# Kernel optimization log

Hardware: AMD Instinct MI355X
Metric: run time of the kernel (lower is better)

Reference implementation:

```python
import jax, jax.numpy as jnp
import numpy as np

B, PD, CD = 8192, 1024, 1024


def setup_inputs() -> dict:
    key = jax.random.key(0)
    ks = jax.random.split(key, 10)
    u = lambda k, shape: jax.random.uniform(k, shape, dtype=jnp.float32, minval=-0.05, maxval=0.05)
    return {
        "P": jax.random.normal(ks[0], (B, PD), dtype=jnp.float32),
        "C1": jax.random.normal(ks[1], (B, CD), dtype=jnp.float32),
        "C2": jax.random.normal(ks[2], (B, CD), dtype=jnp.float32),
        "C3": jax.random.normal(ks[3], (B, CD), dtype=jnp.float32),
        "C4": jax.random.normal(ks[4], (B, CD), dtype=jnp.float32),
        "GateWeight_P": u(ks[5], (PD, CD)),
        "GateWeight_C": u(ks[6], (CD, CD)),
        "GateBias": u(ks[7], (CD,)),
        "OutWeight": u(ks[8], (PD, CD)),
        "OutBias": u(ks[9], (CD, 1)),
    }


def reference(P, C1, C2, C3, C4, GateWeight_P, GateWeight_C, GateBias, OutWeight, OutBias):
    # Stack the 4 choice branches: [4, B, C]
    Cs = jnp.stack([C1, C2, C3, C4], axis=0)
    WP = P @ GateWeight_P                                  # [B, C]
    WC = jnp.einsum("kbc,cd->kbd", Cs, GateWeight_C)       # [4, B, C]
    g = jax.nn.sigmoid(WP[None] + WC + GateBias)           # [4, B, C]
    C_dash = Cs * g                                        # [4, B, C]
    WP_out = P @ OutWeight                                 # [B, C]
    scores = jnp.einsum("kbc,bc->kb", C_dash, WP_out)      # batch_dot axes=[1,1]
    bias = jnp.einsum("kbc,c->kb", C_dash, OutBias[:, 0])  # K.dot(C_dash, OutBias)
    return (scores + bias).T                               # [B, 4]
```

## Files before the change

### kernel.cpp

```cpp
#include <hip/hip_runtime.h>
#include <hip/hip_bf16.h>


#define B_  8192
#define PD_ 1024
#define CD_ 1024

typedef unsigned short ushort_t;
typedef __attribute__((ext_vector_type(8))) short    short8;
typedef __attribute__((ext_vector_type(8))) unsigned short ushort8;
typedef __attribute__((ext_vector_type(4))) float    floatx4;

__device__ __forceinline__ float bf2f(unsigned short u) {
    return __uint_as_float(((unsigned)u) << 16);
}
__device__ __forceinline__ unsigned short f2bf(float f) {
    unsigned u = __float_as_uint(f);
    unsigned r = u + 0x7FFFu + ((u >> 16) & 1u);
    return (unsigned short)(r >> 16);
}

__global__ __launch_bounds__(256) void prep_kernel(const float* __restrict__ P,
                                                   const float* __restrict__ C1,
                                                   const float* __restrict__ C2,
                                                   const float* __restrict__ C3,
                                                   const float* __restrict__ C4,
                                                   const float* __restrict__ GWP,
                                                   const float* __restrict__ OW,
                                                   const float* __restrict__ GWC,
                                                   ushort_t* __restrict__ Pb,
                                                   ushort_t* __restrict__ Call,
                                                   ushort_t* __restrict__ Wcat,
                                                   ushort_t* __restrict__ GWCt,
                                                   float* __restrict__ out) {
    const int bid = blockIdx.x;
    const int tid = threadIdx.x;
    if (bid < 40960) {
        const int seg = bid >> 13;
        const int i   = (bid & 8191) * 256 + tid;
        const float* src;
        ushort_t* dst;
        switch (seg) {
            case 0: src = P;  dst = Pb; break;
            case 1: src = C1; dst = Call; break;
            case 2: src = C2; dst = Call + (size_t)1 * B_ * CD_; break;
            case 3: src = C3; dst = Call + (size_t)2 * B_ * CD_; break;
            default: src = C4; dst = Call + (size_t)3 * B_ * CD_; break;
        }
        float4 v = ((const float4*)src)[i];
        ushort4 o;
        o.x = f2bf(v.x); o.y = f2bf(v.y); o.z = f2bf(v.z); o.w = f2bf(v.w);
        ((ushort4*)dst)[i] = o;
    } else if (bid < 44032) {
        __shared__ float tile[32][33];
        const int tb  = bid - 40960;
        const int seg = tb >> 10;
        const int t32 = tb & 1023;
        const float* src;
        ushort_t* dst;
        switch (seg) {
            case 0: src = GWP; dst = Wcat; break;
            case 1: src = OW;  dst = Wcat + 1024 * 1024; break;
            default: src = GWC; dst = GWCt; break;
        }
        const int c0 = (t32 & 31) * 32, r0 = (t32 >> 5) * 32;
        const int x = tid & 31, y = tid >> 5;
        for (int i = y; i < 32; i += 8)
            tile[i][x] = src[(size_t)(r0 + i) * 1024 + c0 + x];
        __syncthreads();
        for (int i = y; i < 32; i += 8)
            dst[(size_t)(c0 + i) * 1024 + r0 + x] = f2bf(tile[x][i]);
    } else {
        const int i = (bid - 44032) * 256 + tid;
        ((float4*)out)[i] = float4{0.f, 0.f, 0.f, 0.f};
    }
}

__device__ __forceinline__ void gl_lds16(const void* g, void* l) {
    __builtin_amdgcn_global_load_lds((const __attribute__((address_space(1))) void*)g,
                                     (__attribute__((address_space(3))) void*)l, 16, 0, 0);
}

__global__ __launch_bounds__(512, 4) void gemmA(const ushort_t* __restrict__ A,
                                                const ushort_t* __restrict__ Bt,
                                                ushort_t* __restrict__ C) {
    __shared__ ushort_t smem[12288];
    ushort_t* lA = smem;
    ushort_t* lB = smem + 4096;
    const int K = 1024, N = 2048;
    const int xcd = blockIdx.x & 7, q = blockIdx.x >> 3;
    const int tileM = ((q >> 3) * 8 + xcd) * 128;
    const int tileN = (q & 7) * 256;

    const int t = threadIdx.x;
    const int wave = t >> 6, lane = t & 63;
    const int quad = lane >> 4, l16 = lane & 15;
    const int wm = wave >> 2, wn = wave & 3;

    const int srow = lane >> 2;
    const int sc   = ((lane & 3) ^ ((lane >> 4) & 3)) * 8;
    const ushort_t* Ag  = A  + (size_t)(tileM + wave * 16 + srow) * K + sc;
    const ushort_t* Bg0 = Bt + (size_t)(tileN + wave * 32 + srow) * K + sc;
    const ushort_t* Bg1 = Bg0 + (size_t)16 * K;
    const int loA = wave * 512 + lane * 8;
    const int loB = wave * 1024 + lane * 8;
    const int fro = (l16 * 4 + (quad ^ (l16 >> 2))) * 8;

    floatx4 acc[4][4];
#pragma unroll
    for (int i = 0; i < 4; i++)
#pragma unroll
        for (int j = 0; j < 4; j++) acc[i][j] = (floatx4)0.f;

    for (int k0 = 0; k0 < K; k0 += 32) {
        gl_lds16(Ag + k0,  &lA[loA]);
        gl_lds16(Bg0 + k0, &lB[loB]);
        gl_lds16(Bg1 + k0, &lB[loB + 512]);
        __syncthreads();
        short8 af[4], bfr[4];
#pragma unroll
        for (int mi = 0; mi < 4; mi++)
            af[mi] = *(const short8*)&lA[(wm * 4 + mi) * 512 + fro];
#pragma unroll
        for (int ni = 0; ni < 4; ni++)
            bfr[ni] = *(const short8*)&lB[(wn * 4 + ni) * 512 + fro];
#pragma unroll
        for (int mi = 0; mi < 4; mi++)
#pragma unroll
            for (int ni = 0; ni < 4; ni++)
                acc[mi][ni] = __builtin_amdgcn_mfma_f32_16x16x32_bf16(
                    af[mi], bfr[ni], acc[mi][ni], 0, 0, 0);
        __syncthreads();
    }
#pragma unroll
    for (int mi = 0; mi < 4; mi++)
#pragma unroll
        for (int ni = 0; ni < 4; ni++)
#pragma unroll
            for (int r = 0; r < 4; r++) {
                int row = tileM + wm * 64 + mi * 16 + quad * 4 + r;
                int col = tileN + wn * 64 + ni * 16 + l16;
                C[(size_t)row * N + col] = f2bf(acc[mi][ni][r]);
            }
}

__global__ __launch_bounds__(512, 4) void gemmB_fused(const ushort_t* __restrict__ Call,
                                                      const ushort_t* __restrict__ GWCt,
                                                      const ushort_t* __restrict__ WPcat,
                                                      const float* __restrict__ Gb,
                                                      const float* __restrict__ Ob,
                                                      float* __restrict__ out) {
    __shared__ ushort_t smem[12288];
    ushort_t* lA = smem;
    ushort_t* lB = smem + 4096;
    const int K = 1024;
    const int xcd = blockIdx.x & 7, q = blockIdx.x >> 3;
    const int tileM = ((q >> 2) * 8 + xcd) * 128;
    const int tileN = (q & 3) * 256;

    const int t = threadIdx.x;
    const int wave = t >> 6, lane = t & 63;
    const int quad = lane >> 4, l16 = lane & 15;
    const int wm = wave >> 2, wn = wave & 3;

    const int srow = lane >> 2;
    const int sc   = ((lane & 3) ^ ((lane >> 4) & 3)) * 8;
    const ushort_t* Ag  = Call + (size_t)(tileM + wave * 16 + srow) * K + sc;
    const ushort_t* Bg0 = GWCt + (size_t)(tileN + wave * 32 + srow) * K + sc;
    const ushort_t* Bg1 = Bg0 + (size_t)16 * K;
    const int loA = wave * 512 + lane * 8;
    const int loB = wave * 1024 + lane * 8;
    const int fro = (l16 * 4 + (quad ^ (l16 >> 2))) * 8;

    floatx4 acc[4][4];
#pragma unroll
    for (int i = 0; i < 4; i++)
#pragma unroll
        for (int j = 0; j < 4; j++) acc[i][j] = (floatx4)0.f;

    for (int k0 = 0; k0 < K; k0 += 32) {
        gl_lds16(Ag + k0,  &lA[loA]);
        gl_lds16(Bg0 + k0, &lB[loB]);
        gl_lds16(Bg1 + k0, &lB[loB + 512]);
        __syncthreads();
        short8 af[4], bfr[4];
#pragma unroll
        for (int mi = 0; mi < 4; mi++)
            af[mi] = *(const short8*)&lA[(wm * 4 + mi) * 512 + fro];
#pragma unroll
        for (int ni = 0; ni < 4; ni++)
            bfr[ni] = *(const short8*)&lB[(wn * 4 + ni) * 512 + fro];
#pragma unroll
        for (int mi = 0; mi < 4; mi++)
#pragma unroll
            for (int ni = 0; ni < 4; ni++)
                acc[mi][ni] = __builtin_amdgcn_mfma_f32_16x16x32_bf16(
                    af[mi], bfr[ni], acc[mi][ni], 0, 0, 0);
        __syncthreads();
    }

    const int kk   = tileM >> 13;
    const int b0   = (tileM & 8191) + wm * 64 + quad * 4;
    const int rowg = tileM + wm * 64 + quad * 4;

#pragma unroll
    for (int mi = 0; mi < 4; mi++) {
        float part[4] = {0.f, 0.f, 0.f, 0.f};
#pragma unroll
        for (int ni = 0; ni < 4; ni++) {
            const int gcol = tileN + wn * 64 + ni * 16 + l16;
            const float gbv = Gb[gcol];
            const float obv = Ob[gcol];
            const ushort_t* wpp = WPcat + (size_t)(b0 + mi * 16) * 2048 + gcol;
            const ushort_t* ckp = Call  + (size_t)(rowg + mi * 16) * 1024 + gcol;
#pragma unroll
            for (int r = 0; r < 4; r++) {
                float wp  = bf2f(wpp[(size_t)r * 2048]);
                float wpo = bf2f(wpp[(size_t)r * 2048 + 1024]);
                float ck  = bf2f(ckp[(size_t)r * 1024]);
                float x = wp + acc[mi][ni][r] + gbv;
                float g = 1.f / (1.f + __expf(-x));
                part[r] += ck * g * (wpo + obv);
            }
        }
#pragma unroll
        for (int r = 0; r < 4; r++) {
            part[r] += __shfl_xor(part[r], 1);
            part[r] += __shfl_xor(part[r], 2);
            part[r] += __shfl_xor(part[r], 4);
            part[r] += __shfl_xor(part[r], 8);
        }
        if (l16 == 0) {
#pragma unroll
            for (int r = 0; r < 4; r++)
                atomicAdd(&out[(size_t)(b0 + mi * 16 + r) * 4 + kk], part[r]);
        }
    }
}

extern "C" void kernel_launch(void* const* d_in, const int* in_sizes, int n_in,
                              void* d_out, int out_size, void* d_ws, size_t ws_size,
                              hipStream_t stream) {
    (void)in_sizes; (void)n_in; (void)out_size; (void)ws_size;
    const float* P   = (const float*)d_in[0];
    const float* C1  = (const float*)d_in[1];
    const float* C2  = (const float*)d_in[2];
    const float* C3  = (const float*)d_in[3];
    const float* C4  = (const float*)d_in[4];
    const float* GWP = (const float*)d_in[5];
    const float* GWC = (const float*)d_in[6];
    const float* Gb  = (const float*)d_in[7];
    const float* OW  = (const float*)d_in[8];
    const float* Ob  = (const float*)d_in[9];
    float* out = (float*)d_out;

    char* ws = (char*)d_ws;
    ushort_t* Pb    = (ushort_t*)(ws);
    ushort_t* Call  = (ushort_t*)(ws + (16u << 20));
    ushort_t* Wcat  = (ushort_t*)(ws + (80u << 20));
    ushort_t* GWCt  = (ushort_t*)(ws + (84u << 20));
    ushort_t* WPcat = (ushort_t*)(ws + (86u << 20));

    prep_kernel<<<44064, 256, 0, stream>>>(P, C1, C2, C3, C4, GWP, OW, GWC,
                                           Pb, Call, Wcat, GWCt, out);
    gemmA<<<512, 512, 0, stream>>>(Pb, Wcat, WPcat);
    gemmB_fused<<<1024, 512, 0, stream>>>(Call, GWCt, WPcat, Gb, Ob, out);
}
```

Before: 345.0 us.

## Use 256x256 tiles with 4-stage LDS pipeline and interleaved WP pairs

Replaces both GEMMs' 128x256 single-buffered K loop with a shared 256x256 tile routine. It prefetches three K-steps ahead into a 4-slot LDS ring, using vmcnt waits and a single barrier per step, and raises MFMA priority during compute. gemmA now writes WP and WP_out interleaved so the fused epilogue reads one 32-bit word per element instead of two strided loads, and bias loads are hoisted. Larger tiles raise data reuse but halve the number of blocks, lower occupancy to 2 blocks per CU and increase register pressure.

Measured after the change: 356.9 us. +3.5%, slower.

```diff
diff --git a/kernel.cpp b/kernel.cpp
--- a/kernel.cpp
+++ b/kernel.cpp
@@ -7,8 +7,8 @@
 #define CD_ 1024
 
 typedef unsigned short ushort_t;
+typedef unsigned int   uint_t;
 typedef __attribute__((ext_vector_type(8))) short    short8;
-typedef __attribute__((ext_vector_type(8))) unsigned short ushort8;
 typedef __attribute__((ext_vector_type(4))) float    floatx4;
 
 __device__ __forceinline__ float bf2f(unsigned short u) {
@@ -81,146 +81,155 @@
                                      (__attribute__((address_space(3))) void*)l, 16, 0, 0);
 }
 
-__global__ __launch_bounds__(512, 4) void gemmA(const ushort_t* __restrict__ A,
-                                                const ushort_t* __restrict__ Bt,
-                                                ushort_t* __restrict__ C) {
-    __shared__ ushort_t smem[12288];
-    ushort_t* lA = smem;
-    ushort_t* lB = smem + 4096;
-    const int K = 1024, N = 2048;
+#define VM8()  asm volatile("s_waitcnt vmcnt(8)" ::: "memory")
+#define VM4()  asm volatile("s_waitcnt vmcnt(4)" ::: "memory")
+#define VM0()  asm volatile("s_waitcnt vmcnt(0)" ::: "memory")
+#define BARR() __builtin_amdgcn_s_barrier()
+
+__device__ __forceinline__ void gemm256_pipeline(const ushort_t* __restrict__ A,
+                                                 const ushort_t* __restrict__ Bt,
+                                                 int tileM, int tileN,
+                                                 ushort_t* smem,
+                                                 floatx4 (&acc)[8][4]) {
+    const int K = 1024;
+    const int t = threadIdx.x;
+    const int w = t >> 6, lane = t & 63;
+    const int quad = lane >> 4, l16 = lane & 15;
+    const int wm = w >> 2, wn = w & 3;
+
+    const int segg = ((lane & 3) ^ ((lane >> 3) & 3)) * 8;
+    const ushort_t* Ap0 = A  + (size_t)(tileM + w * 16 + (lane >> 2)) * K + segg;
+    const ushort_t* Ap1 = Ap0 + (size_t)128 * K;
+    const ushort_t* Bp0 = Bt + (size_t)(tileN + w * 16 + (lane >> 2)) * K + segg;
+    const ushort_t* Bp1 = Bp0 + (size_t)128 * K;
+    const int lA0 = w * 512 + lane * 8;
+    const int lA1 = lA0 + 4096;
+    const int lB0 = 8192 + lA0;
+    const int lB1 = lB0 + 4096;
+
+    const int xs  = (quad ^ ((l16 >> 1) & 3)) * 8;
+    const int roA = (wm * 128 + l16) * 32 + xs;
+    const int roB = 8192 + (wn * 64 + l16) * 32 + xs;
+
+#pragma unroll
+    for (int i = 0; i < 8; i++)
+#pragma unroll
+        for (int j = 0; j < 4; j++) acc[i][j] = (floatx4)0.f;
+
+#define STAGE(kt) do {                                                       \
+        const int base_ = ((kt) & 3) * 16384; const int k0_ = (kt) * 32;     \
+        gl_lds16(Ap0 + k0_, &smem[base_ + lA0]);                             \
+        gl_lds16(Ap1 + k0_, &smem[base_ + lA1]);                             \
+        gl_lds16(Bp0 + k0_, &smem[base_ + lB0]);                             \
+        gl_lds16(Bp1 + k0_, &smem[base_ + lB1]); } while (0)
+
+#define COMPUTE(kt) do {                                                     \
+        const int base_ = ((kt) & 3) * 16384;                                \
+        short8 af_[8], bf_[4];                                               \
+        _Pragma("unroll")                                                    \
+        for (int mi = 0; mi < 8; mi++)                                       \
+            af_[mi] = *(const short8*)&smem[base_ + roA + mi * 512];         \
+        _Pragma("unroll")                                                    \
+        for (int ni = 0; ni < 4; ni++)                                       \
+            bf_[ni] = *(const short8*)&smem[base_ + roB + ni * 512];         \
+        __builtin_amdgcn_s_setprio(1);                                       \
+        _Pragma("unroll")                                                    \
+        for (int mi = 0; mi < 8; mi++)                                       \
+        _Pragma("unroll")                                                    \
+        for (int ni = 0; ni < 4; ni++)                                       \
+            acc[mi][ni] = __builtin_amdgcn_mfma_f32_16x16x32_bf16(           \
+                af_[mi], bf_[ni], acc[mi][ni], 0, 0, 0);                     \
+        __builtin_amdgcn_s_setprio(0); } while (0)
+
+    STAGE(0); STAGE(1); STAGE(2);
+#pragma unroll 4
+    for (int kt = 0; kt < 28; ++kt) {
+        VM8(); BARR();
+        STAGE(kt + 3);
+        COMPUTE(kt);
+    }
+    VM8(); BARR(); STAGE(31); COMPUTE(28);
+    VM8(); BARR(); COMPUTE(29);
+    VM4(); BARR(); COMPUTE(30);
+    VM0(); BARR(); COMPUTE(31);
+#undef STAGE
+#undef COMPUTE
+}
+
+__global__ __launch_bounds__(512, 2) void gemmA_k(const ushort_t* __restrict__ A,
+                                                  const ushort_t* __restrict__ Bt,
+                                                  ushort_t* __restrict__ C) {
+    __shared__ ushort_t smem[65536];
     const int xcd = blockIdx.x & 7, q = blockIdx.x >> 3;
-    const int tileM = ((q >> 3) * 8 + xcd) * 128;
+    const int tileM = ((q >> 3) * 8 + xcd) * 256;
     const int tileN = (q & 7) * 256;
 
-    const int t = threadIdx.x;
-    const int wave = t >> 6, lane = t & 63;
-    const int quad = lane >> 4, l16 = lane & 15;
-    const int wm = wave >> 2, wn = wave & 3;
-
-    const int srow = lane >> 2;
-    const int sc   = ((lane & 3) ^ ((lane >> 4) & 3)) * 8;
-    const ushort_t* Ag  = A  + (size_t)(tileM + wave * 16 + srow) * K + sc;
-    const ushort_t* Bg0 = Bt + (size_t)(tileN + wave * 32 + srow) * K + sc;
-    const ushort_t* Bg1 = Bg0 + (size_t)16 * K;
-    const int loA = wave * 512 + lane * 8;
-    const int loB = wave * 1024 + lane * 8;
-    const int fro = (l16 * 4 + (quad ^ (l16 >> 2))) * 8;
-
-    floatx4 acc[4][4];
-#pragma unroll
-    for (int i = 0; i < 4; i++)
-#pragma unroll
-        for (int j = 0; j < 4; j++) acc[i][j] = (floatx4)0.f;
-
-    for (int k0 = 0; k0 < K; k0 += 32) {
-        gl_lds16(Ag + k0,  &lA[loA]);
-        gl_lds16(Bg0 + k0, &lB[loB]);
-        gl_lds16(Bg1 + k0, &lB[loB + 512]);
-        __syncthreads();
-        short8 af[4], bfr[4];
-#pragma unroll
-        for (int mi = 0; mi < 4; mi++)
-            af[mi] = *(const short8*)&lA[(wm * 4 + mi) * 512 + fro];
-#pragma unroll
-        for (int ni = 0; ni < 4; ni++)
-            bfr[ni] = *(const short8*)&lB[(wn * 4 + ni) * 512 + fro];
-#pragma unroll
-        for (int mi = 0; mi < 4; mi++)
-#pragma unroll
-            for (int ni = 0; ni < 4; ni++)
-                acc[mi][ni] = __builtin_amdgcn_mfma_f32_16x16x32_bf16(
-                    af[mi], bfr[ni], acc[mi][ni], 0, 0, 0);
-        __syncthreads();
-    }
-#pragma unroll
-    for (int mi = 0; mi < 4; mi++)
-#pragma unroll
-        for (int ni = 0; ni < 4; ni++)
+    floatx4 acc[8][4];
+    gemm256_pipeline(A, Bt, tileM, tileN, smem, acc);
+
+    const int t = threadIdx.x, lane = t & 63, quad = lane >> 4, l16 = lane & 15;
+    const int w = t >> 6, wm = w >> 2, wn = w & 3;
+    const int rowb = tileM + wm * 128 + quad * 4;
+#pragma unroll
+    for (int mi = 0; mi < 8; mi++)
+#pragma unroll
+        for (int ni = 0; ni < 4; ni++) {
+            const int col = tileN + wn * 64 + ni * 16 + l16;
+            const int ci = col & 1023, hi = col >> 10;
 #pragma unroll
             for (int r = 0; r < 4; r++) {
-                int row = tileM + wm * 64 + mi * 16 + quad * 4 + r;
-                int col = tileN + wn * 64 + ni * 16 + l16;
-                C[(size_t)row * N + col] = f2bf(acc[mi][ni][r]);
+                const int row = rowb + mi * 16 + r;
+                C[(size_t)(row * 1024 + ci) * 2 + hi] = f2bf(acc[mi][ni][r]);
             }
-}
-
-__global__ __launch_bounds__(512, 4) void gemmB_fused(const ushort_t* __restrict__ Call,
+        }
+}
+
+__global__ __launch_bounds__(512, 2) void gemmB_fused(const ushort_t* __restrict__ Call,
                                                       const ushort_t* __restrict__ GWCt,
-                                                      const ushort_t* __restrict__ WPcat,
+                                                      const uint_t* __restrict__ WPcat,
                                                       const float* __restrict__ Gb,
                                                       const float* __restrict__ Ob,
                                                       float* __restrict__ out) {
-    __shared__ ushort_t smem[12288];
-    ushort_t* lA = smem;
-    ushort_t* lB = smem + 4096;
-    const int K = 1024;
+    __shared__ ushort_t smem[65536];
     const int xcd = blockIdx.x & 7, q = blockIdx.x >> 3;
-    const int tileM = ((q >> 2) * 8 + xcd) * 128;
+    const int tileM = ((q >> 2) * 8 + xcd) * 256;
     const int tileN = (q & 3) * 256;
 
-    const int t = threadIdx.x;
-    const int wave = t >> 6, lane = t & 63;
-    const int quad = lane >> 4, l16 = lane & 15;
-    const int wm = wave >> 2, wn = wave & 3;
-
-    const int srow = lane >> 2;
-    const int sc   = ((lane & 3) ^ ((lane >> 4) & 3)) * 8;
-    const ushort_t* Ag  = Call + (size_t)(tileM + wave * 16 + srow) * K + sc;
-    const ushort_t* Bg0 = GWCt + (size_t)(tileN + wave * 32 + srow) * K + sc;
-    const ushort_t* Bg1 = Bg0 + (size_t)16 * K;
-    const int loA = wave * 512 + lane * 8;
-    const int loB = wave * 1024 + lane * 8;
-    const int fro = (l16 * 4 + (quad ^ (l16 >> 2))) * 8;
-
-    floatx4 acc[4][4];
-#pragma unroll
-    for (int i = 0; i < 4; i++)
-#pragma unroll
-        for (int j = 0; j < 4; j++) acc[i][j] = (floatx4)0.f;
-
-    for (int k0 = 0; k0 < K; k0 += 32) {
-        gl_lds16(Ag + k0,  &lA[loA]);
-        gl_lds16(Bg0 + k0, &lB[loB]);
-        gl_lds16(Bg1 + k0, &lB[loB + 512]);
-        __syncthreads();
-        short8 af[4], bfr[4];
-#pragma unroll
-        for (int mi = 0; mi < 4; mi++)
-            af[mi] = *(const short8*)&lA[(wm * 4 + mi) * 512 + fro];
-#pragma unroll
-        for (int ni = 0; ni < 4; ni++)
-            bfr[ni] = *(const short8*)&lB[(wn * 4 + ni) * 512 + fro];
-#pragma unroll
-        for (int mi = 0; mi < 4; mi++)
-#pragma unroll
-            for (int ni = 0; ni < 4; ni++)
-                acc[mi][ni] = __builtin_amdgcn_mfma_f32_16x16x32_bf16(
-                    af[mi], bfr[ni], acc[mi][ni], 0, 0, 0);
-        __syncthreads();
-    }
-
-    const int kk   = tileM >> 13;
-    const int b0   = (tileM & 8191) + wm * 64 + quad * 4;
-    const int rowg = tileM + wm * 64 + quad * 4;
-
-#pragma unroll
-    for (int mi = 0; mi < 4; mi++) {
+    floatx4 acc[8][4];
+    gemm256_pipeline(Call, GWCt, tileM, tileN, smem, acc);
+
+    const int t = threadIdx.x, lane = t & 63, quad = lane >> 4, l16 = lane & 15;
+    const int w = t >> 6, wm = w >> 2, wn = w & 3;
+
+    const int kk    = tileM >> 13;
+    const int b0    = (tileM & 8191) + wm * 128 + quad * 4;
+    const int rowg0 = tileM + wm * 128 + quad * 4;
+
+    float gbv[4], obv[4];
+    int   gcol[4];
+#pragma unroll
+    for (int ni = 0; ni < 4; ni++) {
+        gcol[ni] = tileN + wn * 64 + ni * 16 + l16;
+        gbv[ni]  = Gb[gcol[ni]];
+        obv[ni]  = Ob[gcol[ni]];
+    }
+
+#pragma unroll
+    for (int mi = 0; mi < 8; mi++) {
         float part[4] = {0.f, 0.f, 0.f, 0.f};
 #pragma unroll
         for (int ni = 0; ni < 4; ni++) {
-            const int gcol = tileN + wn * 64 + ni * 16 + l16;
-            const float gbv = Gb[gcol];
-            const float obv = Ob[gcol];
-            const ushort_t* wpp = WPcat + (size_t)(b0 + mi * 16) * 2048 + gcol;
-            const ushort_t* ckp = Call  + (size_t)(rowg + mi * 16) * 1024 + gcol;
+            const uint_t*   wpp = WPcat + (size_t)(b0 + mi * 16) * 1024 + gcol[ni];
+            const ushort_t* ckp = Call  + (size_t)(rowg0 + mi * 16) * 1024 + gcol[ni];
 #pragma unroll
             for (int r = 0; r < 4; r++) {
-                float wp  = bf2f(wpp[(size_t)r * 2048]);
-                float wpo = bf2f(wpp[(size_t)r * 2048 + 1024]);
-                float ck  = bf2f(ckp[(size_t)r * 1024]);
-                float x = wp + acc[mi][ni][r] + gbv;
-                float g = 1.f / (1.f + __expf(-x));
-                part[r] += ck * g * (wpo + obv);
+                const uint_t wpair = wpp[(size_t)r * 1024];
+                const float wp  = bf2f((unsigned short)(wpair & 0xffffu));
+                const float wpo = bf2f((unsigned short)(wpair >> 16));
+                const float ck  = bf2f(ckp[(size_t)r * 1024]);
+                const float x = wp + acc[mi][ni][r] + gbv[ni];
+                const float g = 1.f / (1.f + __expf(-x));
+                part[r] += ck * g * (wpo + obv[ni]);
             }
         }
 #pragma unroll
@@ -263,6 +272,6 @@
 
     prep_kernel<<<44064, 256, 0, stream>>>(P, C1, C2, C3, C4, GWP, OW, GWC,
                                            Pb, Call, Wcat, GWCt, out);
-    gemmA<<<512, 512, 0, stream>>>(Pb, Wcat, WPcat);
-    gemmB_fused<<<1024, 512, 0, stream>>>(Call, GWCt, WPcat, Gb, Ob, out);
-}
+    gemmA_k<<<256, 512, 0, stream>>>(Pb, Wcat, WPcat);
+    gemmB_fused<<<512, 512, 0, stream>>>(Call, GWCt, (const uint_t*)WPcat, Gb, Ob, out);
+}
```

## Interleave WP/WPout outputs as bf16 pairs and retune LDS swizzle

Applied to the files above, without the earlier changes.

gemmA now writes WP and WP_out interleaved per column, so the fused epilogue of gemmB reads both values with a single 32-bit load instead of two scattered 16-bit loads. The LDS XOR swizzle used for global-to-LDS staging and fragment reads changes to a different lane-bit pattern to reduce bank conflicts. Bias loads are hoisted out of the mi loop. The interleaved stores in gemmA become strided 2-byte writes, which may coalesce less well.

New measurement: 345.4 us. About the same (+0.1%).

```diff
diff --git a/kernel.cpp b/kernel.cpp
--- a/kernel.cpp
+++ b/kernel.cpp
@@ -7,8 +7,8 @@
 #define CD_ 1024
 
 typedef unsigned short ushort_t;
+typedef unsigned int   uint_t;
 typedef __attribute__((ext_vector_type(8))) short    short8;
-typedef __attribute__((ext_vector_type(8))) unsigned short ushort8;
 typedef __attribute__((ext_vector_type(4))) float    floatx4;
 
 __device__ __forceinline__ float bf2f(unsigned short u) {
@@ -87,7 +87,7 @@
     __shared__ ushort_t smem[12288];
     ushort_t* lA = smem;
     ushort_t* lB = smem + 4096;
-    const int K = 1024, N = 2048;
+    const int K = 1024;
     const int xcd = blockIdx.x & 7, q = blockIdx.x >> 3;
     const int tileM = ((q >> 3) * 8 + xcd) * 128;
     const int tileN = (q & 7) * 256;
@@ -98,13 +98,13 @@
     const int wm = wave >> 2, wn = wave & 3;
 
     const int srow = lane >> 2;
-    const int sc   = ((lane & 3) ^ ((lane >> 4) & 3)) * 8;
+    const int sc   = ((lane & 3) ^ ((lane >> 3) & 3)) * 8;
     const ushort_t* Ag  = A  + (size_t)(tileM + wave * 16 + srow) * K + sc;
     const ushort_t* Bg0 = Bt + (size_t)(tileN + wave * 32 + srow) * K + sc;
     const ushort_t* Bg1 = Bg0 + (size_t)16 * K;
     const int loA = wave * 512 + lane * 8;
     const int loB = wave * 1024 + lane * 8;
-    const int fro = (l16 * 4 + (quad ^ (l16 >> 2))) * 8;
+    const int fro = (l16 * 4 + (quad ^ ((l16 >> 1) & 3))) * 8;
 
     floatx4 acc[4][4];
 #pragma unroll
@@ -135,18 +135,20 @@
 #pragma unroll
     for (int mi = 0; mi < 4; mi++)
 #pragma unroll
-        for (int ni = 0; ni < 4; ni++)
+        for (int ni = 0; ni < 4; ni++) {
+            const int col = tileN + wn * 64 + ni * 16 + l16;
+            const int ci = col & 1023, hi = col >> 10;
 #pragma unroll
             for (int r = 0; r < 4; r++) {
-                int row = tileM + wm * 64 + mi * 16 + quad * 4 + r;
-                int col = tileN + wn * 64 + ni * 16 + l16;
-                C[(size_t)row * N + col] = f2bf(acc[mi][ni][r]);
+                const int row = tileM + wm * 64 + mi * 16 + quad * 4 + r;
+                C[(size_t)(row * 1024 + ci) * 2 + hi] = f2bf(acc[mi][ni][r]);
             }
+        }
 }
 
 __global__ __launch_bounds__(512, 4) void gemmB_fused(const ushort_t* __restrict__ Call,
                                                       const ushort_t* __restrict__ GWCt,
-                                                      const ushort_t* __restrict__ WPcat,
+                                                      const uint_t* __restrict__ WPcat,
                                                       const float* __restrict__ Gb,
                                                       const float* __restrict__ Ob,
                                                       float* __restrict__ out) {
@@ -164,13 +166,13 @@
     const int wm = wave >> 2, wn = wave & 3;
 
     const int srow = lane >> 2;
-    const int sc   = ((lane & 3) ^ ((lane >> 4) & 3)) * 8;
+    const int sc   = ((lane & 3) ^ ((lane >> 3) & 3)) * 8;
     const ushort_t* Ag  = Call + (size_t)(tileM + wave * 16 + srow) * K + sc;
     const ushort_t* Bg0 = GWCt + (size_t)(tileN + wave * 32 + srow) * K + sc;
     const ushort_t* Bg1 = Bg0 + (size_t)16 * K;
     const int loA = wave * 512 + lane * 8;
     const int loB = wave * 1024 + lane * 8;
-    const int fro = (l16 * 4 + (quad ^ (l16 >> 2))) * 8;
+    const int fro = (l16 * 4 + (quad ^ ((l16 >> 1) & 3))) * 8;
 
     floatx4 acc[4][4];
 #pragma unroll
@@ -203,24 +205,31 @@
     const int b0   = (tileM & 8191) + wm * 64 + quad * 4;
     const int rowg = tileM + wm * 64 + quad * 4;
 
+    float gbv[4], obv[4];
+    int   gcol[4];
+#pragma unroll
+    for (int ni = 0; ni < 4; ni++) {
+        gcol[ni] = tileN + wn * 64 + ni * 16 + l16;
+        gbv[ni]  = Gb[gcol[ni]];
+        obv[ni]  = Ob[gcol[ni]];
+    }
+
 #pragma unroll
     for (int mi = 0; mi < 4; mi++) {
         float part[4] = {0.f, 0.f, 0.f, 0.f};
 #pragma unroll
         for (int ni = 0; ni < 4; ni++) {
-            const int gcol = tileN + wn * 64 + ni * 16 + l16;
-            const float gbv = Gb[gcol];
-            const float obv = Ob[gcol];
-            const ushort_t* wpp = WPcat + (size_t)(b0 + mi * 16) * 2048 + gcol;
-            const ushort_t* ckp = Call  + (size_t)(rowg + mi * 16) * 1024 + gcol;
+            const uint_t*   wpp = WPcat + (size_t)(b0 + mi * 16) * 1024 + gcol[ni];
+            const ushort_t* ckp = Call  + (size_t)(rowg + mi * 16) * 1024 + gcol[ni];
 #pragma unroll
             for (int r = 0; r < 4; r++) {
-                float wp  = bf2f(wpp[(size_t)r * 2048]);
-                float wpo = bf2f(wpp[(size_t)r * 2048 + 1024]);
-                float ck  = bf2f(ckp[(size_t)r * 1024]);
-                float x = wp + acc[mi][ni][r] + gbv;
-                float g = 1.f / (1.f + __expf(-x));
-                part[r] += ck * g * (wpo + obv);
+                const uint_t wpair = wpp[(size_t)r * 1024];
+                const float wp  = bf2f((unsigned short)(wpair & 0xffffu));
+                const float wpo = bf2f((unsigned short)(wpair >> 16));
+                const float ck  = bf2f(ckp[(size_t)r * 1024]);
+                const float x = wp + acc[mi][ni][r] + gbv[ni];
+                const float g = 1.f / (1.f + __expf(-x));
+                part[r] += ck * g * (wpo + obv[ni]);
             }
         }
 #pragma unroll
@@ -264,5 +273,5 @@
     prep_kernel<<<44064, 256, 0, stream>>>(P, C1, C2, C3, C4, GWP, OW, GWC,
                                            Pb, Call, Wcat, GWCt, out);
     gemmA<<<512, 512, 0, stream>>>(Pb, Wcat, WPcat);
-    gemmB_fused<<<1024, 512, 0, stream>>>(Call, GWCt, WPcat, Gb, Ob, out);
-}
+    gemmB_fused<<<1024, 512, 0, stream>>>(Call, GWCt, (const uint_t*)WPcat, Gb, Ob, out);
+}
```
